# Performance work log

Hardware: AMD Instinct MI355X
Metric: run time of the kernel (lower is better)

## Reference

```python
import jax, jax.numpy as jnp
import numpy as np
import math

B, N, D, H, K = 32, 512, 768, 12, 8  # batch, patches, hidden_dim, heads, n_topic_groups
HD = D // H


def setup_inputs() -> dict:
    key = jax.random.key(0)
    ks = jax.random.split(key, 12)
    hidden_states = jax.random.normal(ks[0], (B, N, D), jnp.float32)
    # group ids in 1..K, every group present (required by original sorted-dict indexing)
    tid = jax.random.permutation(ks[1], (jnp.arange(B, dtype=jnp.int64) % K) + 1)
    s = 1.0 / math.sqrt(D)
    def lin(k):
        kw, kb = jax.random.split(k)
        return (jax.random.normal(kw, (D, D), jnp.float32) * s,
                jax.random.normal(kb, (D,), jnp.float32) * s)
    Wq, bq = lin(ks[2])
    Wk, bk = lin(ks[3])
    Wv, bv = lin(ks[4])
    Wo, bo = lin(ks[5])
    Wc, bc = lin(ks[6])  # Conv1d(D, D, kernel_size=1) == pointwise linear
    return dict(hidden_states=hidden_states, tid=tid, Wq=Wq, bq=bq, Wk=Wk, bk=bk,
                Wv=Wv, bv=bv, Wo=Wo, bo=bo, Wc=Wc, bc=bc)


def reference(hidden_states, tid, Wq, bq, Wk, bk, Wv, bv, Wo, bo, Wc, bc):
    # --- context(): per-group context_aware + mean, scattered back ---
    # context_aware(x) = mean over group of (x + conv1x1(x)); conv is pointwise so
    # it commutes with grouping -> compute per-sample then segment-mean.
    y = hidden_states + jnp.einsum('bnd,ed->bne', hidden_states, Wc) + bc  # [B,N,D]
    seg = tid - 1  # ids are 1..K
    sums = jax.ops.segment_sum(y, seg, num_segments=K)                      # [K,N,D]
    counts = jax.ops.segment_sum(jnp.ones((B,), y.dtype), seg, num_segments=K)
    means = sums / jnp.maximum(counts, 1.0)[:, None, None]
    contexts = means[seg] + hidden_states                                   # [B,N,D]

    # --- dual-stage attention (dropout rate 0 / eval mode) ---
    def heads(x):  # [B,N,D] -> [B,H,N,HD]
        return x.reshape(B, N, H, HD).transpose(0, 2, 1, 3)

    q = heads(hidden_states @ Wq.T + bq)
    t = heads(contexts @ Wq.T + bq)  # topic_states also passes through self.query
    k = heads(hidden_states @ Wk.T + bk)
    v = heads(hidden_states @ Wv.T + bv)

    scale = 1.0 / math.sqrt(HD)
    p1 = jax.nn.softmax(jnp.einsum('bhqd,bhkd->bhqk', t, k) * scale, axis=-1)
    v_t = jnp.einsum('bhqk,bhkd->bhqd', p1, v)
    p2 = jax.nn.softmax(jnp.einsum('bhqd,bhkd->bhqk', q, t) * scale, axis=-1)
    ctx = jnp.einsum('bhqk,bhkd->bhqd', p2, v_t)

    ctx = ctx.transpose(0, 2, 1, 3).reshape(B, N, D)
    return ctx @ Wo.T + bo
```

## Files before the change

kernel.cpp:

```cpp
#include <hip/hip_runtime.h>
#include <hip/hip_bf16.h>


typedef __bf16 bf16_t;
typedef __bf16 bf16x8 __attribute__((ext_vector_type(8)));
typedef __bf16 bf16x4 __attribute__((ext_vector_type(4)));
typedef float f32x4 __attribute__((ext_vector_type(4)));

#define B_ 32
#define N_ 512
#define D_ 768
#define H_ 12
#define HD_ 64
#define K_ 8
#define ND_ (N_ * D_)

typedef __attribute__((address_space(1))) unsigned int as1_u32;
typedef __attribute__((address_space(3))) unsigned int as3_u32;

__device__ __forceinline__ void glds16(const void* g, void* l) {
  __builtin_amdgcn_global_load_lds((as1_u32*)g, (as3_u32*)l, 16, 0, 0);
}

__device__ __forceinline__ f32x4 mfma16(bf16x8 a, bf16x8 b, f32x4 c) {
  return __builtin_amdgcn_mfma_f32_16x16x32_bf16(a, b, c, 0, 0, 0);
}

__device__ __forceinline__ bf16x8 addv8(bf16x8 a, bf16x8 b) {
  bf16x8 o;
#pragma unroll
  for (int j = 0; j < 8; ++j) o[j] = (bf16_t)((float)a[j] + (float)b[j]);
  return o;
}

__device__ __forceinline__ int seg_of(const int* tid, int b) {
  const bool is64 = (tid[1] == 0);
  int v = is64 ? (int)((const long long*)tid)[b] : tid[b];
  return v - 1;
}

__device__ __forceinline__ void gemm_core(const bf16_t* __restrict__ A,
                                          const bf16_t* __restrict__ Bw,
                                          char* smem, f32x4 (&acc)[4][4]) {
  const int t = threadIdx.x;
  const int lane = t & 63, w = t >> 6;
  const int quad = lane >> 4, l15 = lane & 15;
  const int r0 = t >> 2;
  const int c0e = (t & 3) * 8;
  const int wbase = w * 1024;
  const int mRow = (w >> 1) * 64, nCol = (w & 1) * 64;

  const bf16_t* ga0 = A + (size_t)r0 * D_ + c0e;
  const bf16_t* ga1 = A + (size_t)(r0 + 64) * D_ + c0e;
  const bf16_t* gb0 = Bw + (size_t)r0 * D_ + c0e;
  const bf16_t* gb1 = Bw + (size_t)(r0 + 64) * D_ + c0e;

  glds16(ga0, smem + wbase);
  glds16(ga1, smem + 4096 + wbase);
  glds16(gb0, smem + 8192 + wbase);
  glds16(gb1, smem + 12288 + wbase);

  for (int kb = 0; kb < 24; ++kb) {
    __syncthreads();
    char* cur = smem + (kb & 1) * 16384;
    char* nxt = smem + ((kb + 1) & 1) * 16384;
    if (kb < 23) {
      const int ko = (kb + 1) * 32;
      glds16(ga0 + ko, nxt + wbase);
      glds16(ga1 + ko, nxt + 4096 + wbase);
      glds16(gb0 + ko, nxt + 8192 + wbase);
      glds16(gb1 + ko, nxt + 12288 + wbase);
    }
    bf16x8 af[4], bfr[4];
#pragma unroll
    for (int mt = 0; mt < 4; ++mt)
      af[mt] = *(const bf16x8*)(cur + (mRow + mt * 16 + l15) * 64 + quad * 16);
#pragma unroll
    for (int nt = 0; nt < 4; ++nt)
      bfr[nt] = *(const bf16x8*)(cur + 8192 + (nCol + nt * 16 + l15) * 64 +
                                 quad * 16);
#pragma unroll
    for (int mt = 0; mt < 4; ++mt)
#pragma unroll
      for (int nt = 0; nt < 4; ++nt)
        acc[mt][nt] = mfma16(af[mt], bfr[nt], acc[mt][nt]);
  }
}

__device__ __forceinline__ void zero_acc(f32x4 (&acc)[4][4]) {
  const f32x4 z = {0.f, 0.f, 0.f, 0.f};
#pragma unroll
  for (int a = 0; a < 4; ++a)
#pragma unroll
    for (int b = 0; b < 4; ++b) acc[a][b] = z;
}

__global__ __launch_bounds__(256) void k_front(
    const float* __restrict__ x, const float* __restrict__ Wq,
    const float* __restrict__ Wk, const float* __restrict__ Wv,
    const float* __restrict__ Wc, const float* __restrict__ Wo,
    const int* __restrict__ tid, bf16_t* __restrict__ Xb,
    bf16_t* __restrict__ Wqb, bf16_t* __restrict__ Wkb,
    bf16_t* __restrict__ Wvb, bf16_t* __restrict__ Wcb,
    bf16_t* __restrict__ Wob, bf16_t* __restrict__ Mx) {
  if (blockIdx.x < 192) {
    const size_t i = ((size_t)blockIdx.x * 256 + threadIdx.x) * 8;
    float acc[K_][8];
    float cnt[K_];
#pragma unroll
    for (int k = 0; k < K_; ++k) {
      cnt[k] = 0.f;
#pragma unroll
      for (int j = 0; j < 8; ++j) acc[k][j] = 0.f;
    }
    const bool is64 = (tid[1] == 0);
    for (int b = 0; b < B_; ++b) {
      const int s = (is64 ? (int)((const long long*)tid)[b] : tid[b]) - 1;
      const float* p = x + (size_t)b * ND_ + i;
      f32x4 y0 = *(const f32x4*)p;
      f32x4 y1 = *(const f32x4*)(p + 4);
#pragma unroll
      for (int k = 0; k < K_; ++k) {
        const float msk = (s == k) ? 1.f : 0.f;
        cnt[k] += msk;
#pragma unroll
        for (int j = 0; j < 4; ++j) {
          acc[k][j] += msk * y0[j];
          acc[k][4 + j] += msk * y1[j];
        }
      }
    }
#pragma unroll
    for (int k = 0; k < K_; ++k) {
      const float inv = 1.f / fmaxf(cnt[k], 1.f);
      bf16x8 o;
#pragma unroll
      for (int j = 0; j < 8; ++j) o[j] = (bf16_t)(acc[k][j] * inv);
      *(bf16x8*)(Mx + (size_t)k * ND_ + i) = o;
    }
    return;
  }
  int bid = blockIdx.x - 192;
  const float* in;
  bf16_t* out;
  if (bid < 6144) {
    in = x; out = Xb;
  } else {
    const int wi = (bid - 6144) / 288;
    bid = (bid - 6144) % 288;
    in = wi == 0 ? Wq : wi == 1 ? Wk : wi == 2 ? Wv : wi == 3 ? Wc : Wo;
    out = wi == 0 ? Wqb : wi == 1 ? Wkb : wi == 2 ? Wvb : wi == 3 ? Wcb : Wob;
  }
  const size_t i = ((size_t)bid * 256 + threadIdx.x) * 8;
  f32x4 a = *(const f32x4*)(in + i);
  f32x4 b = *(const f32x4*)(in + i + 4);
  bf16x8 o;
#pragma unroll
  for (int j = 0; j < 4; ++j) { o[j] = (bf16_t)a[j]; o[4 + j] = (bf16_t)b[j]; }
  *(bf16x8*)(out + i) = o;
}

__global__ __launch_bounds__(256) void k_mid(
    const bf16_t* __restrict__ X, const bf16_t* __restrict__ Wq,
    const bf16_t* __restrict__ Wk, const bf16_t* __restrict__ Wv,
    const float* __restrict__ bq, const float* __restrict__ bk,
    const float* __restrict__ bv, bf16_t* __restrict__ Q,
    bf16_t* __restrict__ Kb, bf16_t* __restrict__ V,
    const bf16_t* __restrict__ Mx, const bf16_t* __restrict__ Wcb,
    const float* __restrict__ bc, bf16_t* __restrict__ Mb) {
  __shared__ alignas(16) char smem[32768];
  const int lane = threadIdx.x & 63, w = threadIdx.x >> 6;
  const int quad = lane >> 4, l15 = lane & 15;

  if (blockIdx.x < 192) {
    const int mblk = blockIdx.x / 6, nblk = blockIdx.x % 6;
    f32x4 acc[4][4];
    zero_acc(acc);
    gemm_core(Mx + (size_t)mblk * 128 * D_, Wcb + (size_t)nblk * 128 * D_,
              smem, acc);
    const int mbase = mblk * 128 + (w >> 1) * 64;
    const int nbase = nblk * 128 + (w & 1) * 64;
#pragma unroll
    for (int nt = 0; nt < 4; ++nt) {
      const int col = nbase + nt * 16 + l15;
      const float bb = bc[col];
#pragma unroll
      for (int mt = 0; mt < 4; ++mt)
#pragma unroll
        for (int r = 0; r < 4; ++r) {
          const int row = mbase + mt * 16 + quad * 4 + r;
          const size_t oi = (size_t)row * D_ + col;
          Mb[oi] = (bf16_t)(acc[mt][nt][r] + bb + (float)Mx[oi]);
        }
    }
    return;
  }

  const int qbid = blockIdx.x - 192;
  const int xcd = qbid & 7, i = qbid >> 3;
  const int tile = i % 18, rowblk = (i / 18) * 8 + xcd;
  const int wsel = tile / 6, nb = tile % 6;
  const bf16_t* W = wsel == 0 ? Wq : wsel == 1 ? Wk : Wv;
  const float* bias = wsel == 0 ? bq : wsel == 1 ? bk : bv;
  bf16_t* Out = wsel == 0 ? Q : wsel == 1 ? Kb : V;

  f32x4 acc[4][4];
  zero_acc(acc);
  gemm_core(X + (size_t)rowblk * 128 * D_, W + (size_t)nb * 128 * D_, smem,
            acc);

  const int mbase = rowblk * 128 + (w >> 1) * 64;
  const int nbase = nb * 128 + (w & 1) * 64;
#pragma unroll
  for (int nt = 0; nt < 4; ++nt) {
    const int col = nbase + nt * 16 + l15;
    const float bb = bias[col];
#pragma unroll
    for (int mt = 0; mt < 4; ++mt)
#pragma unroll
      for (int r = 0; r < 4; ++r) {
        const int row = mbase + mt * 16 + quad * 4 + r;
        Out[(size_t)row * D_ + col] = (bf16_t)(acc[mt][nt][r] + bb);
      }
  }
}

__global__ __launch_bounds__(256) void k_gemm_plain(
    const bf16_t* __restrict__ A, const bf16_t* __restrict__ W,
    const float* __restrict__ bias, const bf16_t* __restrict__ addA,
    void* __restrict__ Out, int outF32, int swz) {
  __shared__ alignas(16) char smem[32768];
  int mblk, nblk;
  if (swz) {
    const int bid = blockIdx.x;
    const int xcd = bid & 7, i = bid >> 3;
    nblk = i % 6;
    mblk = (i / 6) * 8 + xcd;
  } else {
    mblk = blockIdx.x;
    nblk = blockIdx.y;
  }
  f32x4 acc[4][4];
  zero_acc(acc);
  gemm_core(A + (size_t)mblk * 128 * D_, W + (size_t)nblk * 128 * D_, smem,
            acc);
  const int lane = threadIdx.x & 63, w = threadIdx.x >> 6;
  const int quad = lane >> 4, l15 = lane & 15;
  const int mbase = mblk * 128 + (w >> 1) * 64;
  const int nbase = nblk * 128 + (w & 1) * 64;
#pragma unroll
  for (int nt = 0; nt < 4; ++nt) {
    const int col = nbase + nt * 16 + l15;
    const float bb = bias ? bias[col] : 0.f;
#pragma unroll
    for (int mt = 0; mt < 4; ++mt)
#pragma unroll
      for (int r = 0; r < 4; ++r) {
        const int row = mbase + mt * 16 + quad * 4 + r;
        float v = acc[mt][nt][r] + bb;
        if (addA) v += (float)addA[(size_t)row * D_ + col];
        const size_t oi = (size_t)row * D_ + col;
        if (outF32) ((float*)Out)[oi] = v;
        else ((bf16_t*)Out)[oi] = (bf16_t)v;
      }
  }
}

__global__ __launch_bounds__(256) void k_attn(const bf16_t* __restrict__ Qp,
                                              const bf16_t* __restrict__ Kp,
                                              const bf16_t* __restrict__ Vp,
                                              const bf16_t* __restrict__ Madd,
                                              const int* __restrict__ tid,
                                              bf16_t* __restrict__ Op,
                                              int addq) {
  __shared__ alignas(16) __bf16 Kt[64][72];
  __shared__ alignas(16) __bf16 Vt[64][72];
  __shared__ alignas(16) __bf16 Pl[4][32][72];

  const int lane = threadIdx.x & 63, w = threadIdx.x >> 6;
  const int quad = lane >> 4, l15 = lane & 15;
  const int b = blockIdx.y / H_, h = blockIdx.y % H_;
  const int q0 = blockIdx.x * 128 + w * 32;
  const size_t base = (size_t)b * ND_ + h * HD_;
  const float C = 0.18033688011112042f;
  const int sg = seg_of(tid, b);
  const bf16_t* Mh = Madd + (size_t)sg * ND_ + h * HD_;

  bf16x8 aq[2][2];
#pragma unroll
  for (int mt = 0; mt < 2; ++mt)
#pragma unroll
    for (int ks = 0; ks < 2; ++ks) {
      const size_t off = (size_t)(q0 + mt * 16 + l15) * D_ + ks * 32 + quad * 8;
      bf16x8 q = *(const bf16x8*)(Qp + base + off);
      if (addq == 1) q = addv8(q, *(const bf16x8*)(Mh + off));
      aq[mt][ks] = q;
    }

  f32x4 O[2][4];
  float lacc[2][4];
  {
    const f32x4 z = {0.f, 0.f, 0.f, 0.f};
#pragma unroll
    for (int mt = 0; mt < 2; ++mt)
#pragma unroll
      for (int nt = 0; nt < 4; ++nt) O[mt][nt] = z;
#pragma unroll
    for (int mt = 0; mt < 2; ++mt)
#pragma unroll
      for (int r = 0; r < 4; ++r) lacc[mt][r] = 0.f;
  }

  const int sr = threadIdx.x >> 2, sc = threadIdx.x & 3;
  const int sig_sr = ((sr & 15) << 2) | (sr >> 4);

  bf16x8 kr[2], vr[2];
#pragma unroll
  for (int half = 0; half < 2; ++half) {
    const int cc = sc + half * 4;
    const size_t off = (size_t)sr * D_ + cc * 8;
    bf16x8 kv = *(const bf16x8*)(Kp + base + off);
    if (addq == 2) kv = addv8(kv, *(const bf16x8*)(Mh + off));
    kr[half] = kv;
    vr[half] = *(const bf16x8*)(Vp + base + off);
  }

  for (int c0 = 0; c0 < N_; c0 += 64) {
    __syncthreads();
#pragma unroll
    for (int half = 0; half < 2; ++half) {
      const int cc = sc + half * 4;
      *(bf16x8*)(&Kt[sr][cc * 8]) = kr[half];
#pragma unroll
      for (int j = 0; j < 8; ++j) Vt[cc * 8 + j][sig_sr] = vr[half][j];
    }
    __syncthreads();

    if (c0 + 64 < N_) {
#pragma unroll
      for (int half = 0; half < 2; ++half) {
        const int cc = sc + half * 4;
        const size_t off = (size_t)(c0 + 64 + sr) * D_ + cc * 8;
        bf16x8 kv = *(const bf16x8*)(Kp + base + off);
        if (addq == 2) kv = addv8(kv, *(const bf16x8*)(Mh + off));
        kr[half] = kv;
        vr[half] = *(const bf16x8*)(Vp + base + off);
      }
    }

    f32x4 S[2][4];
    {
      const f32x4 z = {0.f, 0.f, 0.f, 0.f};
#pragma unroll
      for (int mt = 0; mt < 2; ++mt)
#pragma unroll
        for (int nt = 0; nt < 4; ++nt) S[mt][nt] = z;
    }
#pragma unroll
    for (int ks = 0; ks < 2; ++ks) {
      bf16x8 bk[4];
#pragma unroll
      for (int nt = 0; nt < 4; ++nt)
        bk[nt] = *(const bf16x8*)(&Kt[nt * 16 + l15][ks * 32 + quad * 8]);
#pragma unroll
      for (int mt = 0; mt < 2; ++mt)
#pragma unroll
        for (int nt = 0; nt < 4; ++nt)
          S[mt][nt] = mfma16(aq[mt][ks], bk[nt], S[mt][nt]);
    }

#pragma unroll
    for (int mt = 0; mt < 2; ++mt)
#pragma unroll
      for (int r = 0; r < 4; ++r) {
        bf16x4 pk;
#pragma unroll
        for (int nt = 0; nt < 4; ++nt) {
          const float p = exp2f(S[mt][nt][r] * C);
          lacc[mt][r] += p;
          pk[nt] = (bf16_t)p;
        }
        *(bf16x4*)(&Pl[w][mt * 16 + quad * 4 + r][l15 * 4]) = pk;
      }

#pragma unroll
    for (int ks2 = 0; ks2 < 2; ++ks2) {
      bf16x8 ap[2], bv[4];
#pragma unroll
      for (int mt = 0; mt < 2; ++mt)
        ap[mt] = *(const bf16x8*)(&Pl[w][mt * 16 + l15][ks2 * 32 + quad * 8]);
#pragma unroll
      for (int nt2 = 0; nt2 < 4; ++nt2)
        bv[nt2] = *(const bf16x8*)(&Vt[nt2 * 16 + l15][ks2 * 32 + quad * 8]);
#pragma unroll
      for (int mt = 0; mt < 2; ++mt)
#pragma unroll
        for (int nt2 = 0; nt2 < 4; ++nt2)
          O[mt][nt2] = mfma16(ap[mt], bv[nt2], O[mt][nt2]);
    }
  }

#pragma unroll
  for (int mt = 0; mt < 2; ++mt)
#pragma unroll
    for (int r = 0; r < 4; ++r) {
      float l = lacc[mt][r];
#pragma unroll
      for (int d = 1; d < 16; d <<= 1) l += __shfl_xor(l, d);
      const float inv = 1.f / l;
      const size_t row = base + (size_t)(q0 + mt * 16 + quad * 4 + r) * D_;
#pragma unroll
      for (int nt2 = 0; nt2 < 4; ++nt2)
        Op[row + nt2 * 16 + l15] = (bf16_t)(O[mt][nt2][r] * inv);
    }
}

__global__ __launch_bounds__(256) void k_zero(float* __restrict__ out) {
  const size_t i = ((size_t)blockIdx.x * 256 + threadIdx.x) * 8;
  f32x4 z = {0.f, 0.f, 0.f, 0.f};
  *(f32x4*)(out + i) = z;
  *(f32x4*)(out + i + 4) = z;
}

extern "C" void kernel_launch(void* const* d_in, const int* in_sizes, int n_in,
                              void* d_out, int out_size, void* d_ws,
                              size_t ws_size, hipStream_t stream) {
  const float* x  = (const float*)d_in[0];
  const int*  tid = (const int*)d_in[1];
  const float* Wq = (const float*)d_in[2];
  const float* bq = (const float*)d_in[3];
  const float* Wk = (const float*)d_in[4];
  const float* bk = (const float*)d_in[5];
  const float* Wv = (const float*)d_in[6];
  const float* bv = (const float*)d_in[7];
  const float* Wo = (const float*)d_in[8];
  const float* bo = (const float*)d_in[9];
  const float* Wc = (const float*)d_in[10];
  const float* bc = (const float*)d_in[11];

  const size_t SZ  = (size_t)B_ * ND_ * sizeof(bf16_t);
  const size_t MSZ = (size_t)K_ * ND_ * sizeof(bf16_t);
  const size_t WSZ = (size_t)D_ * D_ * sizeof(bf16_t);
  if (ws_size < 3 * SZ + MSZ + 5 * WSZ) {
    k_zero<<<6144, 256, 0, stream>>>((float*)d_out);
    return;
  }

  char* ws = (char*)d_ws;
  bf16_t* Qb  = (bf16_t*)(ws);
  bf16_t* Kb  = (bf16_t*)(ws + SZ);
  bf16_t* Vb  = (bf16_t*)(ws + 2 * SZ);
  bf16_t* Mq  = (bf16_t*)(ws + 3 * SZ);
  bf16_t* Wqb = (bf16_t*)(ws + 3 * SZ + MSZ);
  bf16_t* Wkb = (bf16_t*)(ws + 3 * SZ + MSZ + WSZ);
  bf16_t* Wvb = (bf16_t*)(ws + 3 * SZ + MSZ + 2 * WSZ);
  bf16_t* Wcb = (bf16_t*)(ws + 3 * SZ + MSZ + 3 * WSZ);
  bf16_t* Wob = (bf16_t*)(ws + 3 * SZ + MSZ + 4 * WSZ);
  bf16_t* Mx  = Mq;
  bf16_t* Mb  = (bf16_t*)d_out;
  bf16_t* VT  = (bf16_t*)d_out;
  bf16_t* Xb  = (bf16_t*)d_out + (size_t)B_ * ND_;
  bf16_t* CTX = Kb;

  k_front<<<7776, 256, 0, stream>>>(x, Wq, Wk, Wv, Wc, Wo, tid, Xb, Wqb, Wkb,
                                    Wvb, Wcb, Wob, Mx);
  k_mid<<<2496, 256, 0, stream>>>(Xb, Wqb, Wkb, Wvb, bq, bk, bv, Qb, Kb, Vb,
                                  Mx, Wcb, bc, Mb);
  k_gemm_plain<<<dim3(32, 6), 256, 0, stream>>>(Mb, Wqb, nullptr, nullptr, Mq,
                                                0, 0);
  k_attn<<<dim3(4, B_ * H_), 256, 0, stream>>>(Qb, Kb, Vb, Mq, tid, VT, 1);
  k_attn<<<dim3(4, B_ * H_), 256, 0, stream>>>(Qb, Qb, VT, Mq, tid, CTX, 2);
  k_gemm_plain<<<768, 256, 0, stream>>>(CTX, Wob, bo, nullptr, d_out, 1, 1);
}
```

Before: 416.6 us.

## Fuse context-mean Q projection into mid kernel via atomic counter dependency

The separate launch that projects the per-group context means through Wq is folded into the k_mid grid as 192 extra blocks. These blocks spin on a global atomic counter until the 192 conv blocks have published Mb, then run the GEMM. This removes one kernel launch and its tail. The spin-wait relies on the producer blocks being scheduled before the consumers to avoid deadlock, and Mx is moved to a scratch region inside the output buffer so it no longer aliases Mq.

```diff
diff --git a/kernel.cpp b/kernel.cpp
--- a/kernel.cpp
+++ b/kernel.cpp
@@ -102,14 +102,16 @@
     const int* __restrict__ tid, bf16_t* __restrict__ Xb,
     bf16_t* __restrict__ Wqb, bf16_t* __restrict__ Wkb,
     bf16_t* __restrict__ Wvb, bf16_t* __restrict__ Wcb,
-    bf16_t* __restrict__ Wob, bf16_t* __restrict__ Mx) {
+    bf16_t* __restrict__ Wob, bf16_t* __restrict__ Mx,
+    unsigned* __restrict__ cnt) {
   if (blockIdx.x < 192) {
+    if (blockIdx.x == 0 && threadIdx.x == 0) *cnt = 0u;
     const size_t i = ((size_t)blockIdx.x * 256 + threadIdx.x) * 8;
     float acc[K_][8];
-    float cnt[K_];
+    float cntk[K_];
 #pragma unroll
     for (int k = 0; k < K_; ++k) {
-      cnt[k] = 0.f;
+      cntk[k] = 0.f;
 #pragma unroll
       for (int j = 0; j < 8; ++j) acc[k][j] = 0.f;
     }
@@ -122,7 +124,7 @@
 #pragma unroll
       for (int k = 0; k < K_; ++k) {
         const float msk = (s == k) ? 1.f : 0.f;
-        cnt[k] += msk;
+        cntk[k] += msk;
 #pragma unroll
         for (int j = 0; j < 4; ++j) {
           acc[k][j] += msk * y0[j];
@@ -132,7 +134,7 @@
     }
 #pragma unroll
     for (int k = 0; k < K_; ++k) {
-      const float inv = 1.f / fmaxf(cnt[k], 1.f);
+      const float inv = 1.f / fmaxf(cntk[k], 1.f);
       bf16x8 o;
 #pragma unroll
       for (int j = 0; j < 8; ++j) o[j] = (bf16_t)(acc[k][j] * inv);
@@ -167,7 +169,8 @@
     const float* __restrict__ bv, bf16_t* __restrict__ Q,
     bf16_t* __restrict__ Kb, bf16_t* __restrict__ V,
     const bf16_t* __restrict__ Mx, const bf16_t* __restrict__ Wcb,
-    const float* __restrict__ bc, bf16_t* __restrict__ Mb) {
+    const float* __restrict__ bc, bf16_t* __restrict__ Mb,
+    bf16_t* __restrict__ Mq, unsigned* __restrict__ cnt) {
   __shared__ alignas(16) char smem[32768];
   const int lane = threadIdx.x & 63, w = threadIdx.x >> 6;
   const int quad = lane >> 4, l15 = lane & 15;
@@ -191,6 +194,37 @@
           const int row = mbase + mt * 16 + quad * 4 + r;
           const size_t oi = (size_t)row * D_ + col;
           Mb[oi] = (bf16_t)(acc[mt][nt][r] + bb + (float)Mx[oi]);
+        }
+    }
+    __threadfence();
+    __syncthreads();
+    if (threadIdx.x == 0) atomicAdd(cnt, 1u);
+    return;
+  }
+
+  if (blockIdx.x >= 2496) {
+    const int gbid = blockIdx.x - 2496;
+    const int mblk = gbid / 6, nblk = gbid % 6;
+    if (threadIdx.x == 0) {
+      while (atomicAdd(cnt, 0u) < 192u) __builtin_amdgcn_s_sleep(2);
+    }
+    __syncthreads();
+    __threadfence();
+    f32x4 acc[4][4];
+    zero_acc(acc);
+    gemm_core(Mb + (size_t)mblk * 128 * D_, Wq  + (size_t)nblk * 128 * D_,
+              smem, acc);
+    const int mbase = mblk * 128 + (w >> 1) * 64;
+    const int nbase = nblk * 128 + (w & 1) * 64;
+#pragma unroll
+    for (int nt = 0; nt < 4; ++nt) {
+      const int col = nbase + nt * 16 + l15;
+#pragma unroll
+      for (int mt = 0; mt < 4; ++mt)
+#pragma unroll
+        for (int r = 0; r < 4; ++r) {
+          const int row = mbase + mt * 16 + quad * 4 + r;
+          Mq[(size_t)row * D_ + col] = (bf16_t)acc[mt][nt][r];
         }
     }
     return;
@@ -456,18 +490,17 @@
   bf16_t* Wvb = (bf16_t*)(ws + 3 * SZ + MSZ + 2 * WSZ);
   bf16_t* Wcb = (bf16_t*)(ws + 3 * SZ + MSZ + 3 * WSZ);
   bf16_t* Wob = (bf16_t*)(ws + 3 * SZ + MSZ + 4 * WSZ);
-  bf16_t* Mx  = Mq;
-  bf16_t* Mb  = (bf16_t*)d_out;
-  bf16_t* VT  = (bf16_t*)d_out;
-  bf16_t* Xb  = (bf16_t*)d_out + (size_t)B_ * ND_;
-  bf16_t* CTX = Kb;
+  bf16_t*  Mb  = (bf16_t*)d_out;
+  bf16_t*  Mx  = (bf16_t*)((char*)d_out + 7 * 1024 * 1024);
+  unsigned* cnt = (unsigned*)((char*)d_out + 20 * 1024 * 1024);
+  bf16_t*  VT  = (bf16_t*)d_out;
+  bf16_t*  Xb  = (bf16_t*)d_out + (size_t)B_ * ND_;
+  bf16_t*  CTX = Kb;
 
   k_front<<<7776, 256, 0, stream>>>(x, Wq, Wk, Wv, Wc, Wo, tid, Xb, Wqb, Wkb,
-                                    Wvb, Wcb, Wob, Mx);
-  k_mid<<<2496, 256, 0, stream>>>(Xb, Wqb, Wkb, Wvb, bq, bk, bv, Qb, Kb, Vb,
-                                  Mx, Wcb, bc, Mb);
-  k_gemm_plain<<<dim3(32, 6), 256, 0, stream>>>(Mb, Wqb, nullptr, nullptr, Mq,
-                                                0, 0);
+                                    Wvb, Wcb, Wob, Mx, cnt);
+  k_mid<<<2688, 256, 0, stream>>>(Xb, Wqb, Wkb, Wvb, bq, bk, bv, Qb, Kb, Vb,
+                                  Mx, Wcb, bc, Mb, Mq, cnt);
   k_attn<<<dim3(4, B_ * H_), 256, 0, stream>>>(Qb, Kb, Vb, Mq, tid, VT, 1);
   k_attn<<<dim3(4, B_ * H_), 256, 0, stream>>>(Qb, Qb, VT, Mq, tid, CTX, 2);
   k_gemm_plain<<<768, 256, 0, stream>>>(CTX, Wob, bo, nullptr, d_out, 1, 1);
```

After: 463.0 us. 1.11x slower.
